# Kernel optimization log

Hardware: AMD Instinct MI355X
Metric: run time of the kernel (lower is better)

The kernel has to match this reference:

```python
import jax, jax.numpy as jnp
import numpy as np

TOPK = 13
N_CLASSES = 80
EPS = 1e-9
IOU_EPS = 1e-7


def _make_anchors():
    # YOLOv8 640x640, strides 8/16/32 -> 8400 anchor points (pixel coords, cell centers)
    pts, strides = [], []
    for s in (8, 16, 32):
        n = 640 // s
        c = (np.arange(n, dtype=np.float32) + 0.5) * s
        xs, ys = np.meshgrid(c, c)
        pts.append(np.stack([xs.ravel(), ys.ravel()], -1))
        strides.append(np.full((n * n, 1), s, np.float32))
    return np.concatenate(pts).astype(np.float32), np.concatenate(strides)


def setup_inputs() -> dict:
    key = jax.random.key(0)
    k1, k2, k3, k4, k5 = jax.random.split(key, 5)
    B, G, C = 64, 32, N_CLASSES
    anc, strd = _make_anchors()
    A = anc.shape[0]  # 8400
    # positive l,t,r,b distances so decoded pred boxes are valid
    dist = jnp.abs(jax.random.normal(k1, (B, 4, A))) * 16.0 + 1.0
    cls = jax.random.normal(k2, (B, C, A))
    preds = jnp.concatenate([dist, cls], axis=1)  # (B, 4+C, A)
    x1y1 = jax.random.uniform(k3, (B, G, 2)) * 560.0
    wh = jax.random.uniform(k4, (B, G, 2)) * 64.0 + 8.0
    gt_bboxes = jnp.concatenate([x1y1, x1y1 + wh], axis=-1)  # (B, G, 4) xyxy
    gt_classes = jax.random.randint(k5, (B, G), 0, C)
    return {"preds": preds, "gt_bboxes": gt_bboxes, "gt_classes": gt_classes,
            "anchor_points": jnp.asarray(anc), "stride_tensor": jnp.asarray(strd)}


def _iou_xyxy(a, b):
    # a: (B,A,1,4), b: (B,1,G,4) -> (B,A,G)
    lt = jnp.maximum(a[..., :2], b[..., :2])
    rb = jnp.minimum(a[..., 2:], b[..., 2:])
    wh = jnp.clip(rb - lt, 0.0)
    inter = wh[..., 0] * wh[..., 1]
    area_a = (a[..., 2] - a[..., 0]) * (a[..., 3] - a[..., 1])
    area_b = (b[..., 2] - b[..., 0]) * (b[..., 3] - b[..., 1])
    return inter / (area_a + area_b - inter + IOU_EPS)


def _assign(preds, gt_bboxes, gt_classes, anchor_points, stride_tensor):
    B, G, _ = gt_bboxes.shape
    A = anchor_points.shape[0]
    dist = jnp.transpose(preds[:, :4, :], (0, 2, 1))       # (B,A,4) l,t,r,b
    pred_cls = jnp.transpose(preds[:, 4:, :], (0, 2, 1))    # (B,A,C)
    # dist2bbox (xyxy)
    pb = jnp.concatenate([anchor_points[None] - dist[..., :2],
                          anchor_points[None] + dist[..., 2:]], axis=-1)  # (B,A,4)
    ious = _iou_xyxy(pb[:, :, None, :], gt_bboxes[:, None, :, :])          # (B,A,G)
    probs = jax.nn.softmax(pred_cls, axis=-1)                              # (B,A,C)
    idx_cls = jnp.broadcast_to(gt_classes[:, None, :], (B, A, G))
    cls_score = jnp.take_along_axis(probs, idx_cls, axis=-1)               # (B,A,G)
    align = jnp.sqrt(jnp.maximum(ious, 1e-12)) * jnp.sqrt(jnp.maximum(cls_score, 1e-12))
    # top-k over anchors (dim=1) -> scatter boolean mask
    mt = jnp.transpose(align, (0, 2, 1))                                   # (B,G,A)
    _, idx = jax.lax.top_k(mt, TOPK)                                       # (B,G,TOPK)
    bi = jnp.arange(B)[:, None, None]
    gi = jnp.arange(G)[None, :, None]
    mask = jnp.zeros((B, G, A), bool).at[bi, gi, idx].set(True)
    mask = jnp.transpose(mask, (0, 2, 1))                                  # (B,A,G)
    # anchors inside gt boxes
    d = jnp.concatenate([anchor_points[None, :, None, :] - gt_bboxes[:, None, :, :2],
                         gt_bboxes[:, None, :, 2:] - anchor_points[None, :, None, :]], axis=-1)
    mask = mask & (jnp.min(d, axis=-1) > EPS)
    # anchors assigned to multiple gts keep the highest-IoU gt
    multi = mask.sum(-1) > 1                                               # (B,A)
    best = jnp.argmax(ious, axis=-1)[..., None] == jnp.arange(G)[None, None, :]
    mask = jnp.where(multi[..., None], best, mask)
    fg = mask.any(-1)                                                      # (B,A)
    tgt_idx = jnp.argmax(mask, axis=-1)                                    # (B,A)
    tb = jnp.take_along_axis(gt_bboxes, tgt_idx[..., None], axis=1) * fg[..., None].astype(gt_bboxes.dtype)
    tc = jnp.where(fg, jnp.take_along_axis(gt_classes, tgt_idx, axis=1), 0)
    ts = jnp.take_along_axis(align, tgt_idx[..., None], axis=2)[..., 0] * fg.astype(align.dtype)
    return tb, tc, ts, fg, fg.sum()


def reference(preds, gt_bboxes, gt_classes, anchor_points, stride_tensor):
    return _assign(preds, gt_bboxes, gt_classes, anchor_points, stride_tensor)
```

## Files before the change

### kernel.cpp

```cpp
#include <hip/hip_runtime.h>
#include <cfloat>
#include <cstdint>

#define NB 64
#define NG 32
#define NC 80
#define NA 8400
#define KTOP 13
#define CHUNK 256
#define NCH 33
#define NCAND (NCH * KTOP)
#define GGRP 16

#define CE(ka, ia, kb, ib)                                            \
    {                                                                 \
        const bool sw = (ka < kb) || (ka == kb && ia > ib);           \
        const unsigned tk = sw ? kb : ka;                             \
        const int      ti = sw ? ib : ia;                             \
        kb = sw ? ka : kb;  ib = sw ? ia : ib;                        \
        ka = tk;            ia = ti;                                  \
    }

__device__ __forceinline__ int wave_max_pos(int m) {
    m = max(m, __builtin_amdgcn_update_dpp(0, m, 0x111, 0xF, 0xF, true));
    m = max(m, __builtin_amdgcn_update_dpp(0, m, 0x112, 0xF, 0xF, true));
    m = max(m, __builtin_amdgcn_update_dpp(0, m, 0x114, 0xF, 0xF, true));
    m = max(m, __builtin_amdgcn_update_dpp(0, m, 0x118, 0xF, 0xF, true));
    m = max(m, __builtin_amdgcn_update_dpp(0, m, 0x142, 0xF, 0xF, true));
    m = max(m, __builtin_amdgcn_update_dpp(0, m, 0x143, 0xF, 0xF, true));
    return __builtin_amdgcn_readlane(m, 63);
}

__global__ __launch_bounds__(256) void fusedAB(
    const float* __restrict__ preds,
    const float* __restrict__ gt_bboxes,
    const int*   __restrict__ gt_classes,
    const float* __restrict__ anchor_points,
    float4*      __restrict__ pb_ws,
    float2*      __restrict__ aux_ws,
    unsigned*    __restrict__ inside32,
    int*         __restrict__ bestg,
    float*       __restrict__ candv,
    int*         __restrict__ candi,
    float*       __restrict__ out_sum)
{
    __shared__ float sx1[NG], sy1[NG], sx2[NG], sy2[NG], sarea[NG];
    __shared__ int   scls[NG];
    __shared__ float salign[GGRP][CHUNK];

    const int tid   = threadIdx.x;
    const int chunk = blockIdx.x;
    const int b     = blockIdx.y;
    const int abase = chunk * CHUNK;
    const int a0    = abase + tid;
    const bool live = (a0 < NA);

    if (tid < NG) {
        const float* gb = gt_bboxes + ((size_t)b * NG + tid) * 4;
        const float x1 = gb[0], y1 = gb[1], x2 = gb[2], y2 = gb[3];
        sx1[tid] = x1; sy1[tid] = y1; sx2[tid] = x2; sy2[tid] = y2;
        sarea[tid] = (x2 - x1) * (y2 - y1);
        scls[tid]  = gt_classes[b * NG + tid];
    }
    if (b == 0 && chunk == 0 && tid == 0) out_sum[0] = 0.0f;
    __syncthreads();

    float ax=0, ay=0, x1=0, y1=0, x2=0, y2=0, area=0, mx=0, rd=0;
    const float* cb = nullptr;
    if (live) {
        const float2 ap = *(const float2*)(anchor_points + (size_t)a0 * 2);
        ax = ap.x; ay = ap.y;

        const float* db = preds + (size_t)b * (4 + NC) * NA + a0;
        const float l  = db[0];
        const float t  = db[(size_t)NA];
        const float r  = db[(size_t)2 * NA];
        const float bo = db[(size_t)3 * NA];
        x1 = ax - l; y1 = ay - t; x2 = ax + r; y2 = ay + bo;
        area = (x2 - x1) * (y2 - y1);

        cb = db + (size_t)4 * NA;
        mx = -FLT_MAX;
#pragma unroll 8
        for (int c = 0; c < NC; ++c) mx = fmaxf(mx, cb[(size_t)c * NA]);
        float d = 0.0f;
#pragma unroll 8
        for (int c = 0; c < NC; ++c) d += __expf(cb[(size_t)c * NA] - mx);
        rd = 1.0f / d;
    }

    unsigned ins = 0u;
    int   bg = 0;
    float bi = -1.0f;

    const int lane = tid & 63;
    const int wid  = tid >> 6;

    for (int grp = 0; grp < 2; ++grp) {
        if (live) {
            for (int gg = 0; gg < GGRP; ++gg) {
                const int g = grp * GGRP + gg;
                const float bx1 = sx1[g], by1 = sy1[g], bx2 = sx2[g], by2 = sy2[g];
                const float sag = sarea[g];
                const float cvl = cb[(size_t)scls[g] * NA];
                const float ltx = fmaxf(x1, bx1), lty = fmaxf(y1, by1);
                const float rbx = fminf(x2, bx2), rby = fminf(y2, by2);
                const float w = fmaxf(rbx - ltx, 0.0f), h = fmaxf(rby - lty, 0.0f);
                const float inter = w * h;
                const float iou = inter / (area + sag - inter + 1e-7f);
                if (iou > bi) { bi = iou; bg = g; }
                const float cv = __expf(cvl - mx) * rd;
                const float al = sqrtf(fmaxf(iou, 1e-12f)) * sqrtf(fmaxf(cv, 1e-12f));
                const float dmin = fminf(fminf(ax - bx1, ay - by1), fminf(bx2 - ax, by2 - ay));
                if (dmin > 1e-9f) ins |= (1u << g);
                salign[gg][tid] = al;
            }
        } else {
            for (int gg = 0; gg < GGRP; ++gg) salign[gg][tid] = 0.0f;
        }
        __syncthreads();

        for (int gi = 0; gi < 4; ++gi) {
            const int gg = wid * 4 + gi;
            const int g  = grp * GGRP + gg;

            const float4 q = *(const float4*)&salign[gg][lane * 4];
            unsigned k0 = __float_as_uint(q.x), k1 = __float_as_uint(q.y);
            unsigned k2 = __float_as_uint(q.z), k3 = __float_as_uint(q.w);
            int i0 = abase + lane * 4, i1 = i0 + 1, i2 = i0 + 2, i3 = i0 + 3;

            CE(k0, i0, k2, i2); CE(k1, i1, k3, i3);
            CE(k0, i0, k1, i1); CE(k2, i2, k3, i3);
            CE(k1, i1, k2, i2);

            unsigned rvk = 0u;
            int      ri  = 0x7FFFFFFF;
#pragma unroll
            for (int r = 0; r < KTOP; ++r) {
                const unsigned m = (unsigned)wave_max_pos((int)k0);
                const unsigned long long ball = __ballot(k0 == m);
                const int winner = __ffsll(ball) - 1;
                const int widx = __builtin_amdgcn_readlane(i0, winner);
                if (lane == winner) {
                    k0 = k1; i0 = i1; k1 = k2; i1 = i2; k2 = k3; i2 = i3; k3 = 0u;
                }
                if (lane == r) { rvk = m; ri = widx; }
            }
            if (lane < KTOP) {
                const size_t base = ((size_t)(b * NG + g) * NCH + chunk) * KTOP + lane;
                candv[base] = __uint_as_float(rvk);
                candi[base] = ri;
            }
        }
        __syncthreads();
    }

    if (live) {
        const int i = b * NA + a0;
        pb_ws[i]  = make_float4(x1, y1, x2, y2);
        aux_ws[i] = make_float2(mx, rd);
        inside32[i] = ins;
        bestg[i]    = bg;
    }
}

__global__ __launch_bounds__(256) void mergeTopK(
    const float* __restrict__ candv,
    const int*   __restrict__ candi,
    int*         __restrict__ topk13)
{
    const int tid  = threadIdx.x;
    const int lane = tid & 63;
    const int row  = blockIdx.x * 4 + (tid >> 6);
    const size_t base = (size_t)row * NCAND;

    float v[7]; int id[7];
#pragma unroll
    for (int j = 0; j < 7; ++j) { v[j] = -FLT_MAX; id[j] = 0x7FFFFFFF; }
#pragma unroll
    for (int k = 0; k < 7; ++k) {
        const int j0 = lane + 64 * k;
        if (j0 < NCAND) {
            const float x  = candv[base + j0];
            const int   xi = candi[base + j0];
            if (x > v[6] || (x == v[6] && xi < id[6])) {
                int j = 6;
                while (j > 0 && (v[j - 1] < x || (v[j - 1] == x && id[j - 1] > xi))) {
                    v[j] = v[j - 1]; id[j] = id[j - 1]; --j;
                }
                v[j] = x; id[j] = xi;
            }
        }
    }
    int ri = 0x7FFFFFFF;
    int p = 0;
    for (int r = 0; r < KTOP; ++r) {
        const float cvv = (p < 7) ? v[p]  : -FLT_MAX;
        const int   cii = (p < 7) ? id[p] : 0x7FFFFFFF;
        float bv = cvv; int bi = cii;
#pragma unroll
        for (int off = 32; off > 0; off >>= 1) {
            const float ov = __shfl_xor(bv, off, 64);
            const int   oi = __shfl_xor(bi, off, 64);
            if (ov > bv || (ov == bv && oi < bi)) { bv = ov; bi = oi; }
        }
        if (cii == bi && p < 7) ++p;
        if (lane == r) ri = bi;
    }
    if (lane < KTOP) topk13[(size_t)row * KTOP + lane] = ri;
}

__global__ __launch_bounds__(256) void phaseC(
    const float*    __restrict__ gt_bboxes,
    const int*      __restrict__ gt_classes,
    const float*    __restrict__ preds,
    const float4*   __restrict__ pb_ws,
    const float2*   __restrict__ aux_ws,
    const int*      __restrict__ topk13,
    const unsigned* __restrict__ inside32,
    const int*      __restrict__ bestg,
    float*          __restrict__ out)
{
    __shared__ unsigned smask[CHUNK];
    __shared__ float ssum[4];

    const int tid   = threadIdx.x;
    const int b     = blockIdx.y;
    const int abase = blockIdx.x * CHUNK;
    const int a     = abase + tid;

    smask[tid] = 0u;
    __syncthreads();
    for (int j = tid; j < NG * KTOP; j += 256) {
        const int idx = topk13[(size_t)b * NG * KTOP + j];
        const int rel = idx - abase;
        if (rel >= 0 && rel < CHUNK)
            atomicOr(&smask[rel], 1u << (j / KTOP));
    }
    __syncthreads();

    bool fg = false;
    if (a < NA) {
        const int i = b * NA + a;
        unsigned m = smask[tid] & inside32[i];
        const int cnt = __popc(m);

        int tgt;
        if (cnt > 1)       { tgt = bestg[i];     fg = true;  }
        else if (cnt == 1) { tgt = __ffs(m) - 1; fg = true;  }
        else               { tgt = 0;            fg = false; }

        const float f = fg ? 1.0f : 0.0f;
        const float* gb = gt_bboxes + ((size_t)b * NG + tgt) * 4;
        const float gx1 = gb[0], gy1 = gb[1], gx2 = gb[2], gy2 = gb[3];
        *(float4*)(out + (size_t)i * 4) = make_float4(gx1 * f, gy1 * f, gx2 * f, gy2 * f);

        const size_t BA = (size_t)NB * NA;
        out[BA * 4 + i] = fg ? (float)gt_classes[b * NG + tgt] : 0.0f;

        float ts = 0.0f;
        if (fg) {
            const float4 pb = pb_ws[i];
            const float2 ax = aux_ws[i];
            const float areaA = (pb.z - pb.x) * (pb.w - pb.y);
            const float sag   = (gx2 - gx1) * (gy2 - gy1);
            const float ltx = fmaxf(pb.x, gx1), lty = fmaxf(pb.y, gy1);
            const float rbx = fminf(pb.z, gx2), rby = fminf(pb.w, gy2);
            const float w = fmaxf(rbx - ltx, 0.0f), h = fmaxf(rby - lty, 0.0f);
            const float inter = w * h;
            const float iou = inter / (areaA + sag - inter + 1e-7f);
            const int cls = gt_classes[b * NG + tgt];
            const float cv = __expf(preds[(size_t)b * (4 + NC) * NA + (size_t)(4 + cls) * NA + a] - ax.x) * ax.y;
            ts = sqrtf(fmaxf(iou, 1e-12f)) * sqrtf(fmaxf(cv, 1e-12f));
        }
        out[BA * 5 + i] = ts;
        out[BA * 6 + i] = f;
    }

    const unsigned long long ball = __ballot(fg);
    if ((tid & 63) == 0) ssum[tid >> 6] = (float)__popcll(ball);
    __syncthreads();
    if (tid == 0) {
        const float s = ssum[0] + ssum[1] + ssum[2] + ssum[3];
        if (s != 0.0f) atomicAdd(&out[(size_t)NB * NA * 7], s);
    }
}

extern "C" void kernel_launch(void* const* d_in, const int* in_sizes, int n_in,
                              void* d_out, int out_size, void* d_ws, size_t ws_size,
                              hipStream_t stream) {
    const float* preds         = (const float*)d_in[0];
    const float* gt_bboxes     = (const float*)d_in[1];
    const int*   gt_classes    = (const int*)  d_in[2];
    const float* anchor_points = (const float*)d_in[3];

    float* out = (float*)d_out;
    const size_t BA = (size_t)NB * NA;

    char* ws = (char*)d_ws;
    size_t off = 0;
    float4*   pb_ws    = (float4*)(ws + off);   off += BA * sizeof(float4);
    float2*   aux_ws   = (float2*)(ws + off);   off += BA * sizeof(float2);
    unsigned* inside32 = (unsigned*)(ws + off); off += BA * sizeof(unsigned);
    int*      bestg    = (int*)(ws + off);      off += BA * sizeof(int);
    float*    candv    = (float*)(ws + off);    off += (size_t)NB * NG * NCAND * sizeof(float);
    int*      candi    = (int*)(ws + off);      off += (size_t)NB * NG * NCAND * sizeof(int);
    int*      topk13   = (int*)(ws + off);

    fusedAB<<<dim3(NCH, NB), 256, 0, stream>>>(preds, gt_bboxes, gt_classes, anchor_points,
                                               pb_ws, aux_ws, inside32, bestg,
                                               candv, candi, out + BA * 7);

    mergeTopK<<<NB * NG / 4, 256, 0, stream>>>(candv, candi, topk13);

    phaseC<<<dim3(NCH, NB), 256, 0, stream>>>(gt_bboxes, gt_classes, preds,
                                              pb_ws, aux_ws, topk13,
                                              inside32, bestg, out);
}
```

Before: 400.1 us.

## Stage class logits through shared memory with float4 loads and branchless top-k merge

The fused kernel now loads the box distances and class logits cooperatively as float4 tiles into shared memory, reusing the alignment buffer as the staging area, instead of each thread doing strided scalar loads. The two softmax passes each reload the class tiles, which adds several block barriers per tile. The merge kernel replaces its dynamically indexed insertion-sort arrays with named registers and a branchless rank-based insert, so the arrays are not spilled to scratch memory. The per-class gather in the alignment loop still reads global memory directly.

```diff
diff --git a/kernel.cpp b/kernel.cpp
--- a/kernel.cpp
+++ b/kernel.cpp
@@ -11,6 +11,8 @@
 #define NCH 33
 #define NCAND (NCH * KTOP)
 #define GGRP 16
+#define CTILE 16
+#define NTILE 5
 
 #define CE(ka, ia, kb, ib)                                            \
     {                                                                 \
@@ -46,7 +48,8 @@
 {
     __shared__ float sx1[NG], sy1[NG], sx2[NG], sy2[NG], sarea[NG];
     __shared__ int   scls[NG];
-    __shared__ float salign[GGRP][CHUNK];
+    __shared__ __align__(16) float stage[GGRP][CHUNK];
+    __shared__ __align__(16) float sdist[4][CHUNK];
 
     const int tid   = threadIdx.x;
     const int chunk = blockIdx.x;
@@ -63,31 +66,69 @@
         scls[tid]  = gt_classes[b * NG + tid];
     }
     if (b == 0 && chunk == 0 && tid == 0) out_sum[0] = 0.0f;
-    __syncthreads();
-
-    float ax=0, ay=0, x1=0, y1=0, x2=0, y2=0, area=0, mx=0, rd=0;
-    const float* cb = nullptr;
+
+    {
+        const int p = tid >> 6, k = tid & 63;
+        float4 v = make_float4(0.0f, 0.0f, 0.0f, 0.0f);
+        if (abase + 4 * k < NA)
+            v = *(const float4*)(preds + ((size_t)b * (4 + NC) + p) * NA + abase + 4 * k);
+        *(float4*)&sdist[p][4 * k] = v;
+    }
+    __syncthreads();
+
+    float ax = 0, ay = 0, x1 = 0, y1 = 0, x2 = 0, y2 = 0, area = 0;
     if (live) {
         const float2 ap = *(const float2*)(anchor_points + (size_t)a0 * 2);
         ax = ap.x; ay = ap.y;
-
-        const float* db = preds + (size_t)b * (4 + NC) * NA + a0;
-        const float l  = db[0];
-        const float t  = db[(size_t)NA];
-        const float r  = db[(size_t)2 * NA];
-        const float bo = db[(size_t)3 * NA];
+        const float l  = sdist[0][tid];
+        const float t  = sdist[1][tid];
+        const float r  = sdist[2][tid];
+        const float bo = sdist[3][tid];
         x1 = ax - l; y1 = ay - t; x2 = ax + r; y2 = ay + bo;
         area = (x2 - x1) * (y2 - y1);
-
-        cb = db + (size_t)4 * NA;
-        mx = -FLT_MAX;
-#pragma unroll 8
-        for (int c = 0; c < NC; ++c) mx = fmaxf(mx, cb[(size_t)c * NA]);
-        float d = 0.0f;
-#pragma unroll 8
-        for (int c = 0; c < NC; ++c) d += __expf(cb[(size_t)c * NA] - mx);
-        rd = 1.0f / d;
-    }
+    }
+
+    const float* clsbase = preds + ((size_t)b * (4 + NC) + 4) * NA;
+
+    float mx = -FLT_MAX;
+    for (int t = 0; t < NTILE; ++t) {
+        __syncthreads();
+#pragma unroll
+        for (int i = 0; i < 4; ++i) {
+            const int L = i * 256 + tid;
+            const int p = L >> 6, k = L & 63;
+            float4 v = make_float4(0.0f, 0.0f, 0.0f, 0.0f);
+            if (abase + 4 * k < NA)
+                v = *(const float4*)(clsbase + (size_t)(t * CTILE + p) * NA + abase + 4 * k);
+            ((float4*)&stage[0][0])[L] = v;
+        }
+        __syncthreads();
+        if (live) {
+#pragma unroll
+            for (int c = 0; c < CTILE; ++c) mx = fmaxf(mx, stage[c][tid]);
+        }
+    }
+
+    float d = 0.0f;
+    for (int t = 0; t < NTILE; ++t) {
+        __syncthreads();
+#pragma unroll
+        for (int i = 0; i < 4; ++i) {
+            const int L = i * 256 + tid;
+            const int p = L >> 6, k = L & 63;
+            float4 v = make_float4(0.0f, 0.0f, 0.0f, 0.0f);
+            if (abase + 4 * k < NA)
+                v = *(const float4*)(clsbase + (size_t)(t * CTILE + p) * NA + abase + 4 * k);
+            ((float4*)&stage[0][0])[L] = v;
+        }
+        __syncthreads();
+        if (live) {
+#pragma unroll
+            for (int c = 0; c < CTILE; ++c) d += __expf(stage[c][tid] - mx);
+        }
+    }
+    const float rd = live ? (1.0f / d) : 0.0f;
+    const float* cb = clsbase + a0;
 
     unsigned ins = 0u;
     int   bg = 0;
@@ -95,6 +136,8 @@
 
     const int lane = tid & 63;
     const int wid  = tid >> 6;
+
+    __syncthreads();
 
     for (int grp = 0; grp < 2; ++grp) {
         if (live) {
@@ -113,10 +156,10 @@
                 const float al = sqrtf(fmaxf(iou, 1e-12f)) * sqrtf(fmaxf(cv, 1e-12f));
                 const float dmin = fminf(fminf(ax - bx1, ay - by1), fminf(bx2 - ax, by2 - ay));
                 if (dmin > 1e-9f) ins |= (1u << g);
-                salign[gg][tid] = al;
+                stage[gg][tid] = al;
             }
         } else {
-            for (int gg = 0; gg < GGRP; ++gg) salign[gg][tid] = 0.0f;
+            for (int gg = 0; gg < GGRP; ++gg) stage[gg][tid] = 0.0f;
         }
         __syncthreads();
 
@@ -124,7 +167,7 @@
             const int gg = wid * 4 + gi;
             const int g  = grp * GGRP + gg;
 
-            const float4 q = *(const float4*)&salign[gg][lane * 4];
+            const float4 q = *(const float4*)&stage[gg][lane * 4];
             unsigned k0 = __float_as_uint(q.x), k1 = __float_as_uint(q.y);
             unsigned k2 = __float_as_uint(q.z), k3 = __float_as_uint(q.w);
             int i0 = abase + lane * 4, i1 = i0 + 1, i2 = i0 + 2, i3 = i0 + 3;
@@ -174,38 +217,51 @@
     const int row  = blockIdx.x * 4 + (tid >> 6);
     const size_t base = (size_t)row * NCAND;
 
-    float v[7]; int id[7];
-#pragma unroll
-    for (int j = 0; j < 7; ++j) { v[j] = -FLT_MAX; id[j] = 0x7FFFFFFF; }
+    float v0 = -FLT_MAX, v1 = -FLT_MAX, v2 = -FLT_MAX, v3 = -FLT_MAX,
+          v4 = -FLT_MAX, v5 = -FLT_MAX, v6 = -FLT_MAX;
+    int   d0 = 0x7FFFFFFF, d1 = 0x7FFFFFFF, d2 = 0x7FFFFFFF, d3 = 0x7FFFFFFF,
+          d4 = 0x7FFFFFFF, d5 = 0x7FFFFFFF, d6 = 0x7FFFFFFF;
+
 #pragma unroll
     for (int k = 0; k < 7; ++k) {
         const int j0 = lane + 64 * k;
         if (j0 < NCAND) {
             const float x  = candv[base + j0];
             const int   xi = candi[base + j0];
-            if (x > v[6] || (x == v[6] && xi < id[6])) {
-                int j = 6;
-                while (j > 0 && (v[j - 1] < x || (v[j - 1] == x && id[j - 1] > xi))) {
-                    v[j] = v[j - 1]; id[j] = id[j - 1]; --j;
-                }
-                v[j] = x; id[j] = xi;
-            }
-        }
-    }
+            int r = 0;
+            r += (v0 > x) || (v0 == x && d0 < xi);
+            r += (v1 > x) || (v1 == x && d1 < xi);
+            r += (v2 > x) || (v2 == x && d2 < xi);
+            r += (v3 > x) || (v3 == x && d3 < xi);
+            r += (v4 > x) || (v4 == x && d4 < xi);
+            r += (v5 > x) || (v5 == x && d5 < xi);
+            r += (v6 > x) || (v6 == x && d6 < xi);
+            v6 = (6 < r) ? v6 : ((6 == r) ? x : v5);  d6 = (6 < r) ? d6 : ((6 == r) ? xi : d5);
+            v5 = (5 < r) ? v5 : ((5 == r) ? x : v4);  d5 = (5 < r) ? d5 : ((5 == r) ? xi : d4);
+            v4 = (4 < r) ? v4 : ((4 == r) ? x : v3);  d4 = (4 < r) ? d4 : ((4 == r) ? xi : d3);
+            v3 = (3 < r) ? v3 : ((3 == r) ? x : v2);  d3 = (3 < r) ? d3 : ((3 == r) ? xi : d2);
+            v2 = (2 < r) ? v2 : ((2 == r) ? x : v1);  d2 = (2 < r) ? d2 : ((2 == r) ? xi : d1);
+            v1 = (1 < r) ? v1 : ((1 == r) ? x : v0);  d1 = (1 < r) ? d1 : ((1 == r) ? xi : d0);
+            v0 = (0 == r) ? x  : v0;                  d0 = (0 == r) ? xi : d0;
+        }
+    }
+
     int ri = 0x7FFFFFFF;
-    int p = 0;
-    for (int r = 0; r < KTOP; ++r) {
-        const float cvv = (p < 7) ? v[p]  : -FLT_MAX;
-        const int   cii = (p < 7) ? id[p] : 0x7FFFFFFF;
-        float bv = cvv; int bi = cii;
+#pragma unroll
+    for (int rnd = 0; rnd < KTOP; ++rnd) {
+        float bv = v0; int bi = d0;
 #pragma unroll
         for (int off = 32; off > 0; off >>= 1) {
             const float ov = __shfl_xor(bv, off, 64);
             const int   oi = __shfl_xor(bi, off, 64);
             if (ov > bv || (ov == bv && oi < bi)) { bv = ov; bi = oi; }
         }
-        if (cii == bi && p < 7) ++p;
-        if (lane == r) ri = bi;
+        if (d0 == bi) {
+            v0 = v1; d0 = d1; v1 = v2; d1 = d2; v2 = v3; d2 = d3;
+            v3 = v4; d3 = d4; v4 = v5; d4 = d5; v5 = v6; d5 = d6;
+            v6 = -FLT_MAX; d6 = 0x7FFFFFFF;
+        }
+        if (lane == rnd) ri = bi;
     }
     if (lane < KTOP) topk13[(size_t)row * KTOP + lane] = ri;
 }
```

Result: faster. 388.0 us (-3.0%).
